# Optimization experiments

Measured on AMD Instinct MI355X. Metric: run time of the kernel, lower is better.

Reference implementation:

```python
import jax, jax.numpy as jnp
import numpy as np
from jax.scipy.special import logsumexp

EXPERT_NUM = 64
MOE_TOPK = 2

def setup_inputs() -> dict:
    key = jax.random.key(0)
    k1, k2 = jax.random.split(key)
    x = jax.random.normal(k1, (4, 4096, 4096), dtype=jnp.float32)
    # nn.Linear(input_size, expert_num).weight has shape [expert_num, input_size]
    W = jax.random.normal(k2, (EXPERT_NUM, 4096), dtype=jnp.float32) * (1.0 / np.sqrt(4096))
    return {"x": x, "W": W}

def reference(x, W):
    # logits: [B, S, E]
    logits = jnp.einsum('bsd,ed->bse', x, W)
    k = min(MOE_TOPK + 1, EXPERT_NUM)  # torch takes topk+1 then slices
    topk_logits, topk_indices = jax.lax.top_k(logits, k)
    topk_logits = topk_logits[..., :MOE_TOPK]     # [B, S, K]
    topk_indices = topk_indices[..., :MOE_TOPK]   # [B, S, K]
    # regularized=True: softmax over the top-k logits in float32
    topk_scores = jax.nn.softmax(topk_logits.astype(jnp.float32), axis=-1).astype(logits.dtype)
    # scatter into zeros; topk indices are unique so one-hot sum == scatter-set
    scores_filtered = jnp.sum(
        jax.nn.one_hot(topk_indices, EXPERT_NUM, dtype=logits.dtype) * topk_scores[..., None],
        axis=-2)  # [B, S, E]
    # router_z loss, per-token [B, S]
    log_z = logsumexp(logits, axis=-1)
    loss = log_z ** 2
    return logits, scores_filtered, loss
```

## Files before the change

### kernel.cpp

```cpp
#include <hip/hip_runtime.h>
#include <math.h>

#define TTOK 16384
#define DD   4096
#define EE   64
#define TM   64
#define BK   64
#define KSL  4
#define KW   (DD / KSL)
#define NCHB (KW / BK)

typedef __attribute__((ext_vector_type(8))) short short8;
typedef __attribute__((ext_vector_type(4))) float f32x4;

static __device__ __forceinline__ unsigned short f2bf(float f) {
    unsigned u = __float_as_uint(f);
    u += 0x7FFFu + ((u >> 16) & 1u);
    return (unsigned short)(u >> 16);
}
static __device__ __forceinline__ float bf2f(unsigned short h) {
    return __uint_as_float(((unsigned)h) << 16);
}

static __device__ __forceinline__ void async16(const void* g, void* l) {
    __builtin_amdgcn_global_load_lds(
        (const __attribute__((address_space(1))) unsigned int*)g,
        (__attribute__((address_space(3))) unsigned int*)l, 16, 0, 0);
}

static __device__ __forceinline__ void cvt8(float4 a, float4 b, short8& hi, short8& lo) {
    const float v[8] = {a.x, a.y, a.z, a.w, b.x, b.y, b.z, b.w};
#pragma unroll
    for (int j = 0; j < 8; ++j) {
        const unsigned short h = f2bf(v[j]);
        hi[j] = (short)h;
        lo[j] = (short)f2bf(v[j] - bf2f(h));
    }
}

__global__ void w_convert(const float* __restrict__ W,
                          unsigned short* __restrict__ whi,
                          unsigned short* __restrict__ wlo) {
    const int i = (blockIdx.x * blockDim.x + threadIdx.x) * 4;
    if (i >= EE * DD) return;
    const float4 v = *reinterpret_cast<const float4*>(W + i);
    ushort4 h, l;
    h.x = f2bf(v.x); l.x = f2bf(v.x - bf2f(h.x));
    h.y = f2bf(v.y); l.y = f2bf(v.y - bf2f(h.y));
    h.z = f2bf(v.z); l.z = f2bf(v.z - bf2f(h.z));
    h.w = f2bf(v.w); l.w = f2bf(v.w - bf2f(h.w));
    *reinterpret_cast<ushort4*>(whi + i) = h;
    *reinterpret_cast<ushort4*>(wlo + i) = l;
}

__global__ __launch_bounds__(256, 4)
void gemm_part(const float* __restrict__ x,
               const unsigned short* __restrict__ whi,
               const unsigned short* __restrict__ wlo,
               float* __restrict__ part)
{
    __shared__ float          xs[TM * 64];
    __shared__ unsigned short whs[TM * 64];
    __shared__ unsigned short wls[TM * 64];

    const int tid  = threadIdx.x;
    const int wv   = tid >> 6;
    const int lane = tid & 63;
    const int m    = lane & 15;
    const int q    = lane >> 4;
    const int tile = blockIdx.x & 255;
    const int ks   = blockIdx.x >> 8;
    const int t0   = tile * TM;
    const int k0   = ks * KW;

    const float* gx[4];
#pragma unroll
    for (int i = 0; i < 4; ++i) {
        const int r = 16 * wv + 4 * i + q;
        const int c = m ^ (r & 7);
        gx[i] = x + (size_t)(t0 + r) * DD + k0 + c * 4;
    }
    const unsigned short* gwh[2];
    const unsigned short* gwl[2];
#pragma unroll
    for (int i = 0; i < 2; ++i) {
        const int r = 16 * wv + 8 * i + (lane >> 3);
        const int c = (lane & 7) ^ (r & 7);
        gwh[i] = whi + (size_t)r * DD + k0 + c * 8;
        gwl[i] = wlo + (size_t)r * DD + k0 + c * 8;
    }
    float*          lx[4];
    unsigned short* lwh[2];
    unsigned short* lwl[2];
#pragma unroll
    for (int i = 0; i < 4; ++i) lx[i] = xs + wv * 1024 + i * 256;
#pragma unroll
    for (int i = 0; i < 2; ++i) {
        lwh[i] = whs + wv * 1024 + i * 512;
        lwl[i] = wls + wv * 1024 + i * 512;
    }

    f32x4 acc[4];
#pragma unroll
    for (int e = 0; e < 4; ++e) acc[e] = (f32x4){0.f, 0.f, 0.f, 0.f};

    const int sa = m & 7;
    const int ra = (16 * wv + m) * 64;

    for (int kc = 0; kc < NCHB; ++kc) {
        __syncthreads();
#pragma unroll
        for (int i = 0; i < 4; ++i) async16(gx[i] + kc * BK, lx[i]);
#pragma unroll
        for (int i = 0; i < 2; ++i) {
            async16(gwh[i] + kc * BK, lwh[i]);
            async16(gwl[i] + kc * BK, lwl[i]);
        }
        __syncthreads();

#pragma unroll
        for (int kss = 0; kss < 2; ++kss) {
            const int c0 = 8 * kss + 2 * q;
            const float4 f0 = *reinterpret_cast<const float4*>(xs + ra + ((c0    ) ^ sa) * 4);
            const float4 f1 = *reinterpret_cast<const float4*>(xs + ra + ((c0 + 1) ^ sa) * 4);
            short8 ah, al;
            cvt8(f0, f1, ah, al);
            const int pB = ((4 * kss + q) ^ sa) * 8;
#pragma unroll
            for (int e = 0; e < 4; ++e) {
                const int rb = (16 * e + m) * 64;
                const short8 bh = *reinterpret_cast<const short8*>(whs + rb + pB);
                const short8 bl = *reinterpret_cast<const short8*>(wls + rb + pB);
                acc[e] = __builtin_amdgcn_mfma_f32_16x16x32_bf16(ah, bh, acc[e], 0, 0, 0);
                acc[e] = __builtin_amdgcn_mfma_f32_16x16x32_bf16(ah, bl, acc[e], 0, 0, 0);
                acc[e] = __builtin_amdgcn_mfma_f32_16x16x32_bf16(al, bh, acc[e], 0, 0, 0);
            }
        }
    }

    float* pb = part + ((size_t)ks * TTOK + t0 + 16 * wv + 4 * q) * EE + m;
#pragma unroll
    for (int e = 0; e < 4; ++e)
#pragma unroll
        for (int i = 0; i < 4; ++i)
            pb[(size_t)i * EE + 16 * e] = acc[e][i];
}

__global__ __launch_bounds__(256, 4)
void gate_epi(const float* __restrict__ part, float* __restrict__ out)
{
    __shared__ float lg[TM * 68];
    __shared__ float s1a[TM], s2a[TM];
    __shared__ int   i1a[TM], i2a[TM];

    const int tid = threadIdx.x;
    const int t0  = blockIdx.x * TM;
    const int tt  = tid >> 2;
    const int e0  = (tid & 3) * 16;

    const float* pbase = part + (size_t)(t0 + tt) * EE + e0;
    float4 s[4];
#pragma unroll
    for (int j = 0; j < 4; ++j) s[j] = *reinterpret_cast<const float4*>(pbase + 4 * j);
#pragma unroll
    for (int k = 1; k < KSL; ++k) {
        const float* pk = pbase + (size_t)k * TTOK * EE;
#pragma unroll
        for (int j = 0; j < 4; ++j) {
            const float4 r = *reinterpret_cast<const float4*>(pk + 4 * j);
            s[j].x += r.x; s[j].y += r.y; s[j].z += r.z; s[j].w += r.w;
        }
    }
    float* g = out + (size_t)(t0 + tt) * EE + e0;
    float* lrow = lg + tt * 68 + e0;
#pragma unroll
    for (int j = 0; j < 4; ++j) {
        *reinterpret_cast<float4*>(g + 4 * j)    = s[j];
        *reinterpret_cast<float4*>(lrow + 4 * j) = s[j];
    }
    __syncthreads();

    if (tid < TM) {
        const float* row = lg + tid * 68;
        float v1 = -INFINITY, v2 = -INFINITY;
        int   i1 = 0, i2 = 0;
        for (int e = 0; e < EE; ++e) {
            const float v = row[e];
            if (v > v1)      { v2 = v1; i2 = i1; v1 = v; i1 = e; }
            else if (v > v2) { v2 = v;  i2 = e; }
        }
        float sm = 0.f;
        for (int e = 0; e < EE; ++e) sm += expf(row[e] - v1);
        const float logz = v1 + logf(sm);
        out[(size_t)2 * TTOK * EE + t0 + tid] = logz * logz;
        const float e21 = expf(v2 - v1);
        const float rr  = 1.f / (1.f + e21);
        s1a[tid] = rr; s2a[tid] = e21 * rr; i1a[tid] = i1; i2a[tid] = i2;
    }
    __syncthreads();

    float* sc = out + (size_t)TTOK * EE + (size_t)(t0 + tt) * EE + e0;
    const int i1 = i1a[tt], i2 = i2a[tt];
    const float s1 = s1a[tt], s2 = s2a[tt];
#pragma unroll
    for (int j = 0; j < 4; ++j) {
        float vv[4];
#pragma unroll
        for (int c = 0; c < 4; ++c) {
            const int e = e0 + 4 * j + c;
            vv[c] = (e == i1) ? s1 : ((e == i2) ? s2 : 0.f);
        }
        *reinterpret_cast<float4*>(sc + 4 * j) = make_float4(vv[0], vv[1], vv[2], vv[3]);
    }
}

extern "C" void kernel_launch(void* const* d_in, const int* in_sizes, int n_in,
                              void* d_out, int out_size, void* d_ws, size_t ws_size,
                              hipStream_t stream) {
    const float* x = (const float*)d_in[0];
    const float* W = (const float*)d_in[1];
    float* out = (float*)d_out;
    unsigned short* whi = (unsigned short*)d_ws;
    unsigned short* wlo = whi + (size_t)EE * DD;
    float* part = (float*)(wlo + (size_t)EE * DD);

    w_convert<<<dim3((EE * DD / 4 + 255) / 256), dim3(256), 0, stream>>>(W, whi, wlo);
    gemm_part<<<dim3(256 * KSL), dim3(256), 0, stream>>>(x, whi, wlo, part);
    gate_epi<<<dim3(TTOK / TM), dim3(256), 0, stream>>>(part, out);
}
```

Before: 399.6 us.

## Register-prefetch next K chunk and convert x to bf16 hi/lo before LDS store

Replaces the async global-to-LDS loads with register loads of the next K chunk, issued after the barrier so they overlap the MFMA work on the current chunk. x is split into bf16 hi/lo once when staged into LDS, instead of each wave converting fp32 from LDS, and the LDS footprint stays the same. The cost is more VGPRs for the prefetch buffers, which may lower occupancy under launch bounds of 4 blocks, plus extra VALU conversion on the store path.

```diff
diff --git a/kernel.cpp b/kernel.cpp
--- a/kernel.cpp
+++ b/kernel.cpp
@@ -21,13 +21,6 @@
 static __device__ __forceinline__ float bf2f(unsigned short h) {
     return __uint_as_float(((unsigned)h) << 16);
 }
-
-static __device__ __forceinline__ void async16(const void* g, void* l) {
-    __builtin_amdgcn_global_load_lds(
-        (const __attribute__((address_space(1))) unsigned int*)g,
-        (__attribute__((address_space(3))) unsigned int*)l, 16, 0, 0);
-}
-
 static __device__ __forceinline__ void cvt8(float4 a, float4 b, short8& hi, short8& lo) {
     const float v[8] = {a.x, a.y, a.z, a.w, b.x, b.y, b.z, b.w};
 #pragma unroll
@@ -59,7 +52,8 @@
                const unsigned short* __restrict__ wlo,
                float* __restrict__ part)
 {
-    __shared__ float          xs[TM * 64];
+    __shared__ unsigned short xh[TM * 64];
+    __shared__ unsigned short xl[TM * 64];
     __shared__ unsigned short whs[TM * 64];
     __shared__ unsigned short wls[TM * 64];
 
@@ -73,64 +67,77 @@
     const int t0   = tile * TM;
     const int k0   = ks * KW;
 
-    const float* gx[4];
-#pragma unroll
-    for (int i = 0; i < 4; ++i) {
-        const int r = 16 * wv + 4 * i + q;
-        const int c = m ^ (r & 7);
-        gx[i] = x + (size_t)(t0 + r) * DD + k0 + c * 4;
-    }
-    const unsigned short* gwh[2];
-    const unsigned short* gwl[2];
-#pragma unroll
-    for (int i = 0; i < 2; ++i) {
-        const int r = 16 * wv + 8 * i + (lane >> 3);
-        const int c = (lane & 7) ^ (r & 7);
-        gwh[i] = whi + (size_t)r * DD + k0 + c * 8;
-        gwl[i] = wlo + (size_t)r * DD + k0 + c * 8;
-    }
-    float*          lx[4];
-    unsigned short* lwh[2];
-    unsigned short* lwl[2];
-#pragma unroll
-    for (int i = 0; i < 4; ++i) lx[i] = xs + wv * 1024 + i * 256;
-#pragma unroll
-    for (int i = 0; i < 2; ++i) {
-        lwh[i] = whs + wv * 1024 + i * 512;
-        lwl[i] = wls + wv * 1024 + i * 512;
-    }
+    const int sr = tid >> 3;
+    const int sj = tid & 7;
+    const int sp = (sj ^ (sr & 7)) * 8;
+
+    const float* gx0          = x   + (size_t)(t0 + sr) * DD + k0 + sj * 8;
+    const float* gx1          = gx0 + (size_t)32 * DD;
+    const unsigned short* gh0 = whi + (size_t)sr * DD + k0 + sj * 8;
+    const unsigned short* gh1 = gh0 + (size_t)32 * DD;
+    const unsigned short* gl0 = wlo + (size_t)sr * DD + k0 + sj * 8;
+    const unsigned short* gl1 = gl0 + (size_t)32 * DD;
+
+    unsigned short* const lds_r0 = (unsigned short*)0 + sr * 64 + sp;
+    const int o0 = sr * 64 + sp;
+    const int o1 = (sr + 32) * 64 + sp;
+    (void)lds_r0;
 
     f32x4 acc[4];
 #pragma unroll
     for (int e = 0; e < 4; ++e) acc[e] = (f32x4){0.f, 0.f, 0.f, 0.f};
+
+    float4 fx00 = *reinterpret_cast<const float4*>(gx0);
+    float4 fx01 = *reinterpret_cast<const float4*>(gx0 + 4);
+    float4 fx10 = *reinterpret_cast<const float4*>(gx1);
+    float4 fx11 = *reinterpret_cast<const float4*>(gx1 + 4);
+    short8 pwh0 = *reinterpret_cast<const short8*>(gh0);
+    short8 pwh1 = *reinterpret_cast<const short8*>(gh1);
+    short8 pwl0 = *reinterpret_cast<const short8*>(gl0);
+    short8 pwl1 = *reinterpret_cast<const short8*>(gl1);
 
     const int sa = m & 7;
     const int ra = (16 * wv + m) * 64;
 
     for (int kc = 0; kc < NCHB; ++kc) {
         __syncthreads();
-#pragma unroll
-        for (int i = 0; i < 4; ++i) async16(gx[i] + kc * BK, lx[i]);
-#pragma unroll
-        for (int i = 0; i < 2; ++i) {
-            async16(gwh[i] + kc * BK, lwh[i]);
-            async16(gwl[i] + kc * BK, lwl[i]);
+        {
+            short8 h, l;
+            cvt8(fx00, fx01, h, l);
+            *reinterpret_cast<short8*>(xh + o0) = h;
+            *reinterpret_cast<short8*>(xl + o0) = l;
+            cvt8(fx10, fx11, h, l);
+            *reinterpret_cast<short8*>(xh + o1) = h;
+            *reinterpret_cast<short8*>(xl + o1) = l;
+            *reinterpret_cast<short8*>(whs + o0) = pwh0;
+            *reinterpret_cast<short8*>(whs + o1) = pwh1;
+            *reinterpret_cast<short8*>(wls + o0) = pwl0;
+            *reinterpret_cast<short8*>(wls + o1) = pwl1;
         }
         __syncthreads();
 
+        if (kc + 1 < NCHB) {
+            const int off = (kc + 1) * BK;
+            fx00 = *reinterpret_cast<const float4*>(gx0 + off);
+            fx01 = *reinterpret_cast<const float4*>(gx0 + off + 4);
+            fx10 = *reinterpret_cast<const float4*>(gx1 + off);
+            fx11 = *reinterpret_cast<const float4*>(gx1 + off + 4);
+            pwh0 = *reinterpret_cast<const short8*>(gh0 + off);
+            pwh1 = *reinterpret_cast<const short8*>(gh1 + off);
+            pwl0 = *reinterpret_cast<const short8*>(gl0 + off);
+            pwl1 = *reinterpret_cast<const short8*>(gl1 + off);
+        }
+
 #pragma unroll
         for (int kss = 0; kss < 2; ++kss) {
-            const int c0 = 8 * kss + 2 * q;
-            const float4 f0 = *reinterpret_cast<const float4*>(xs + ra + ((c0    ) ^ sa) * 4);
-            const float4 f1 = *reinterpret_cast<const float4*>(xs + ra + ((c0 + 1) ^ sa) * 4);
-            short8 ah, al;
-            cvt8(f0, f1, ah, al);
-            const int pB = ((4 * kss + q) ^ sa) * 8;
+            const int ca = ((4 * kss + q) ^ sa) * 8;
+            const short8 ah = *reinterpret_cast<const short8*>(xh + ra + ca);
+            const short8 al = *reinterpret_cast<const short8*>(xl + ra + ca);
 #pragma unroll
             for (int e = 0; e < 4; ++e) {
                 const int rb = (16 * e + m) * 64;
-                const short8 bh = *reinterpret_cast<const short8*>(whs + rb + pB);
-                const short8 bl = *reinterpret_cast<const short8*>(wls + rb + pB);
+                const short8 bh = *reinterpret_cast<const short8*>(whs + rb + ca);
+                const short8 bl = *reinterpret_cast<const short8*>(wls + rb + ca);
                 acc[e] = __builtin_amdgcn_mfma_f32_16x16x32_bf16(ah, bh, acc[e], 0, 0, 0);
                 acc[e] = __builtin_amdgcn_mfma_f32_16x16x32_bf16(ah, bl, acc[e], 0, 0, 0);
                 acc[e] = __builtin_amdgcn_mfma_f32_16x16x32_bf16(al, bh, acc[e], 0, 0, 0);
```

Result: no change. 397.6 us (-0.5%).

## Register-prefetch GEMM chunks, use 512-thread blocks, halve K-split count

Applied to the files above, without the earlier changes.

Replaces the async global-to-LDS loads with a register prefetch. The next K chunk is loaded into registers while the current chunk is computed from shared memory, which should overlap global latency with MFMA work. Blocks now hold 8 waves that split the 64 experts into two halves, the K chunk doubles to 128, and the K-split count drops from 4 to 2. That halves the partial-sum traffic but gives half as many blocks and uses more LDS and registers per block.

```diff
diff --git a/kernel.cpp b/kernel.cpp
--- a/kernel.cpp
+++ b/kernel.cpp
@@ -5,10 +5,10 @@
 #define DD   4096
 #define EE   64
 #define TM   64
-#define BK   64
-#define KSL  4
+#define KC   128
+#define KSL  2
 #define KW   (DD / KSL)
-#define NCHB (KW / BK)
+#define NG   (KW / KC)
 
 typedef __attribute__((ext_vector_type(8))) short short8;
 typedef __attribute__((ext_vector_type(4))) float f32x4;
@@ -21,13 +21,6 @@
 static __device__ __forceinline__ float bf2f(unsigned short h) {
     return __uint_as_float(((unsigned)h) << 16);
 }
-
-static __device__ __forceinline__ void async16(const void* g, void* l) {
-    __builtin_amdgcn_global_load_lds(
-        (const __attribute__((address_space(1))) unsigned int*)g,
-        (__attribute__((address_space(3))) unsigned int*)l, 16, 0, 0);
-}
-
 static __device__ __forceinline__ void cvt8(float4 a, float4 b, short8& hi, short8& lo) {
     const float v[8] = {a.x, a.y, a.z, a.w, b.x, b.y, b.z, b.w};
 #pragma unroll
@@ -53,97 +46,108 @@
     *reinterpret_cast<ushort4*>(wlo + i) = l;
 }
 
-__global__ __launch_bounds__(256, 4)
+__global__ __launch_bounds__(512, 4)
 void gemm_part(const float* __restrict__ x,
                const unsigned short* __restrict__ whi,
                const unsigned short* __restrict__ wlo,
                float* __restrict__ part)
 {
-    __shared__ float          xs[TM * 64];
-    __shared__ unsigned short whs[TM * 64];
-    __shared__ unsigned short wls[TM * 64];
+    __shared__ float          xs[TM * KC];
+    __shared__ unsigned short whs[TM * KC];
+    __shared__ unsigned short wls[TM * KC];
 
     const int tid  = threadIdx.x;
     const int wv   = tid >> 6;
     const int lane = tid & 63;
     const int m    = lane & 15;
     const int q    = lane >> 4;
+    const int g    = wv & 3;
+    const int h    = wv >> 2;
     const int tile = blockIdx.x & 255;
-    const int ks   = blockIdx.x >> 8;
+    const int ksb  = blockIdx.x >> 8;
     const int t0   = tile * TM;
-    const int k0   = ks * KW;
-
-    const float* gx[4];
-#pragma unroll
-    for (int i = 0; i < 4; ++i) {
-        const int r = 16 * wv + 4 * i + q;
-        const int c = m ^ (r & 7);
-        gx[i] = x + (size_t)(t0 + r) * DD + k0 + c * 4;
-    }
-    const unsigned short* gwh[2];
-    const unsigned short* gwl[2];
-#pragma unroll
-    for (int i = 0; i < 2; ++i) {
-        const int r = 16 * wv + 8 * i + (lane >> 3);
-        const int c = (lane & 7) ^ (r & 7);
-        gwh[i] = whi + (size_t)r * DD + k0 + c * 8;
-        gwl[i] = wlo + (size_t)r * DD + k0 + c * 8;
-    }
-    float*          lx[4];
-    unsigned short* lwh[2];
-    unsigned short* lwl[2];
-#pragma unroll
-    for (int i = 0; i < 4; ++i) lx[i] = xs + wv * 1024 + i * 256;
-#pragma unroll
-    for (int i = 0; i < 2; ++i) {
-        lwh[i] = whs + wv * 1024 + i * 512;
-        lwl[i] = wls + wv * 1024 + i * 512;
-    }
-
-    f32x4 acc[4];
-#pragma unroll
-    for (int e = 0; e < 4; ++e) acc[e] = (f32x4){0.f, 0.f, 0.f, 0.f};
-
-    const int sa = m & 7;
-    const int ra = (16 * wv + m) * 64;
-
-    for (int kc = 0; kc < NCHB; ++kc) {
+    const int k0   = ksb * KW;
+
+    const int sr = tid >> 3;
+    const int sl = tid & 7;
+    const int sk = sr & 7;
+
+    const float*          gx  = x   + (size_t)(t0 + sr) * DD + k0 + sl * 4;
+    const unsigned short* gwh = whi + (size_t)sr * DD + k0 + sl * 16;
+    const unsigned short* gwl = wlo + (size_t)sr * DD + k0 + sl * 16;
+
+    int xo[4];
+#pragma unroll
+    for (int i = 0; i < 4; ++i) xo[i] = sr * KC + ((sl ^ sk) + 8 * i) * 4;
+    const int wo0 = sr * KC + ((2 * sl    ) ^ sk) * 8;
+    const int wo1 = sr * KC + ((2 * sl + 1) ^ sk) * 8;
+
+    f32x4 acc[2];
+    acc[0] = (f32x4){0.f, 0.f, 0.f, 0.f};
+    acc[1] = (f32x4){0.f, 0.f, 0.f, 0.f};
+
+    float4 px[4];
+    short8 pwh[2], pwl[2];
+#pragma unroll
+    for (int i = 0; i < 4; ++i) px[i] = *reinterpret_cast<const float4*>(gx + 32 * i);
+#pragma unroll
+    for (int b = 0; b < 2; ++b) {
+        pwh[b] = *reinterpret_cast<const short8*>(gwh + 8 * b);
+        pwl[b] = *reinterpret_cast<const short8*>(gwl + 8 * b);
+    }
+
+    const int fk = m & 7;
+    const int ar = (16 * g + m) * KC;
+
+    for (int gen = 0; gen < NG; ++gen) {
         __syncthreads();
 #pragma unroll
-        for (int i = 0; i < 4; ++i) async16(gx[i] + kc * BK, lx[i]);
-#pragma unroll
-        for (int i = 0; i < 2; ++i) {
-            async16(gwh[i] + kc * BK, lwh[i]);
-            async16(gwl[i] + kc * BK, lwl[i]);
-        }
+        for (int i = 0; i < 4; ++i) *reinterpret_cast<float4*>(xs + xo[i]) = px[i];
+        *reinterpret_cast<short8*>(whs + wo0) = pwh[0];
+        *reinterpret_cast<short8*>(whs + wo1) = pwh[1];
+        *reinterpret_cast<short8*>(wls + wo0) = pwl[0];
+        *reinterpret_cast<short8*>(wls + wo1) = pwl[1];
         __syncthreads();
 
-#pragma unroll
-        for (int kss = 0; kss < 2; ++kss) {
-            const int c0 = 8 * kss + 2 * q;
-            const float4 f0 = *reinterpret_cast<const float4*>(xs + ra + ((c0    ) ^ sa) * 4);
-            const float4 f1 = *reinterpret_cast<const float4*>(xs + ra + ((c0 + 1) ^ sa) * 4);
+        if (gen + 1 < NG) {
+            const int off = (gen + 1) * KC;
+#pragma unroll
+            for (int i = 0; i < 4; ++i)
+                px[i] = *reinterpret_cast<const float4*>(gx + off + 32 * i);
+#pragma unroll
+            for (int b = 0; b < 2; ++b) {
+                pwh[b] = *reinterpret_cast<const short8*>(gwh + off + 8 * b);
+                pwl[b] = *reinterpret_cast<const short8*>(gwl + off + 8 * b);
+            }
+        }
+
+#pragma unroll
+        for (int ks = 0; ks < 4; ++ks) {
+            const int p0 = ks * 8 + ((2 * q    ) ^ fk);
+            const int p1 = ks * 8 + ((2 * q + 1) ^ fk);
+            const float4 f0 = *reinterpret_cast<const float4*>(xs + ar + p0 * 4);
+            const float4 f1 = *reinterpret_cast<const float4*>(xs + ar + p1 * 4);
             short8 ah, al;
             cvt8(f0, f1, ah, al);
-            const int pB = ((4 * kss + q) ^ sa) * 8;
-#pragma unroll
-            for (int e = 0; e < 4; ++e) {
-                const int rb = (16 * e + m) * 64;
-                const short8 bh = *reinterpret_cast<const short8*>(whs + rb + pB);
-                const short8 bl = *reinterpret_cast<const short8*>(wls + rb + pB);
-                acc[e] = __builtin_amdgcn_mfma_f32_16x16x32_bf16(ah, bh, acc[e], 0, 0, 0);
-                acc[e] = __builtin_amdgcn_mfma_f32_16x16x32_bf16(ah, bl, acc[e], 0, 0, 0);
-                acc[e] = __builtin_amdgcn_mfma_f32_16x16x32_bf16(al, bh, acc[e], 0, 0, 0);
+#pragma unroll
+            for (int et = 0; et < 2; ++et) {
+                const int br = ((32 * h + 16 * et) + m) * KC;
+                const int pc = (ks * 4 + q) ^ fk;
+                const short8 bh = *reinterpret_cast<const short8*>(whs + br + pc * 8);
+                const short8 bl = *reinterpret_cast<const short8*>(wls + br + pc * 8);
+                acc[et] = __builtin_amdgcn_mfma_f32_16x16x32_bf16(ah, bh, acc[et], 0, 0, 0);
+                acc[et] = __builtin_amdgcn_mfma_f32_16x16x32_bf16(ah, bl, acc[et], 0, 0, 0);
+                acc[et] = __builtin_amdgcn_mfma_f32_16x16x32_bf16(al, bh, acc[et], 0, 0, 0);
             }
         }
     }
 
-    float* pb = part + ((size_t)ks * TTOK + t0 + 16 * wv + 4 * q) * EE + m;
-#pragma unroll
-    for (int e = 0; e < 4; ++e)
+    float* pb = part + ((size_t)ksb * TTOK + t0 + 16 * g + 4 * q) * EE + 32 * h + m;
+#pragma unroll
+    for (int et = 0; et < 2; ++et)
 #pragma unroll
         for (int i = 0; i < 4; ++i)
-            pb[(size_t)i * EE + 16 * e] = acc[e][i];
+            pb[(size_t)i * EE + 16 * et] = acc[et][i];
 }
 
 __global__ __launch_bounds__(256, 4)
@@ -171,11 +175,11 @@
             s[j].x += r.x; s[j].y += r.y; s[j].z += r.z; s[j].w += r.w;
         }
     }
-    float* g = out + (size_t)(t0 + tt) * EE + e0;
+    float* gptr = out + (size_t)(t0 + tt) * EE + e0;
     float* lrow = lg + tt * 68 + e0;
 #pragma unroll
     for (int j = 0; j < 4; ++j) {
-        *reinterpret_cast<float4*>(g + 4 * j)    = s[j];
+        *reinterpret_cast<float4*>(gptr + 4 * j) = s[j];
         *reinterpret_cast<float4*>(lrow + 4 * j) = s[j];
     }
     __syncthreads();
@@ -224,7 +228,7 @@
     unsigned short* wlo = whi + (size_t)EE * DD;
     float* part = (float*)(wlo + (size_t)EE * DD);
 
-    w_convert<<<dim3((EE * DD / 4 + 255) / 256), dim3(256), 0, stream>>>(W, whi, wlo);
-    gemm_part<<<dim3(256 * KSL), dim3(256), 0, stream>>>(x, whi, wlo, part);
+    w_convert<<<dim3(EE * DD / 4 / 256), dim3(256), 0, stream>>>(W, whi, wlo);
+    gemm_part<<<dim3(256 * KSL), dim3(512), 0, stream>>>(x, whi, wlo, part);
     gate_epi<<<dim3(TTOK / TM), dim3(256), 0, stream>>>(part, out);
 }
```

After: 417.6 us. 4.5% more time.
